# Kernel tuning notes

Measured on AMD Instinct MI355X. Metric: run time of the kernel, lower is better.

## Reference

```python
import jax, jax.numpy as jnp
import numpy as np

B, NG, GS, H = 256, 3008, 10, 6          # batch, n_genes, genes per leaf term, hidden per term
T = [2048, 256, 32, 1]                    # terms per DAG level (leaves -> root)
IN = [GS, 8 * H, 8 * H, 32 * H]           # per-term input size at each level
EPS = 1e-5


def setup_inputs() -> dict:
    keys = iter(jax.random.split(jax.random.key(0), 64))

    def rn(shape, s=0.1):
        return jax.random.normal(next(keys), shape, dtype=jnp.float32) * s

    d = {"x": rn((B, NG), 1.0),
         "gW": rn((T[0], GS, NG)),   # stacked leaf direct_gene_layer weights
         "gb": rn((T[0], GS))}
    for l in range(4):
        t, i = T[l], IN[l]
        d[f"w{l}"] = rn((t, H, i))          # term linear weight
        d[f"b{l}"] = rn((t, H))             # term linear bias
        d[f"g{l}"] = jnp.ones((t, H), jnp.float32)   # BN gamma
        d[f"e{l}"] = jnp.zeros((t, H), jnp.float32)  # BN beta
        d[f"p{l}"] = rn((t, H))             # aux linear1 weight (H->1)
        d[f"q{l}"] = rn((t,))               # aux linear1 bias
        d[f"r{l}"] = rn((t,))               # aux linear2 weight (1->1)
        d[f"s{l}"] = rn((t,))               # aux linear2 bias
    d["fw"] = rn((2 * H, H)); d["fb"] = rn((2 * H,))
    d["fg"] = jnp.ones((2 * H,), jnp.float32); d["fe"] = jnp.zeros((2 * H,), jnp.float32)
    d["pw"] = rn((1, 2 * H)); d["pb"] = rn((1,))
    d["rw"] = rn((1, 1)); d["rb"] = rn((1,))
    return d


def _bn(z, g, b):
    # BatchNorm1d in training mode: biased batch stats over axis 0
    m = z.mean(0)
    v = ((z - m) ** 2).mean(0)
    return (z - m) * jax.lax.rsqrt(v + EPS) * g + b


def reference(x, gW, gb,
              w0, b0, g0, e0, p0, q0, r0, s0,
              w1, b1, g1, e1, p1, q1, r1, s1,
              w2, b2, g2, e2, p2, q2, r2, s2,
              w3, b3, g3, e3, p3, q3, r3, s3,
              fw, fb, fg, fe, pw, pb, rw, rb):
    Bn = x.shape[0]
    # stacked direct gene layers for all leaf terms: [B, T0, GS]
    h = jnp.einsum('bn,tgn->btg', x, gW) + gb
    levels = [(w0, b0, g0, e0, p0, q0, r0, s0),
              (w1, b1, g1, e1, p1, q1, r1, s1),
              (w2, b2, g2, e2, p2, q2, r2, s2),
              (w3, b3, g3, e3, p3, q3, r3, s3)]
    aux = []
    for (w, b, g, e, p, q, r, s) in levels:
        # children of term t are contiguous -> concat == reshape
        hin = h.reshape(Bn, w.shape[0], w.shape[2])      # [B, T_l, in_l]
        z = jnp.tanh(jnp.einsum('bti,thi->bth', hin, w) + b)
        y = _bn(z, g, e)                                  # term_NN_out_map
        aux.append(r * jnp.tanh(jnp.einsum('bth,th->bt', y, p) + q) + s)
        h = y
    yroot = h.reshape(Bn, H)                              # root output [B, H]
    of = _bn(jnp.tanh(yroot @ fw.T + fb), fg, fe)         # final BN [B, 2H]
    auxf = jnp.tanh(of @ pw.T + pb) @ rw.T + rb           # final aux [B, 1]
    return jnp.concatenate(aux + [auxf], axis=1)          # [B, 2048+256+32+1+1]
```

## Files before the change

### kernel.cpp

```cpp
#include <hip/hip_runtime.h>
#include <hip/hip_bf16.h>
#include <stdint.h>

#define EPS 1e-5f
#define NOUT 2338

typedef __bf16 bf16x8 __attribute__((ext_vector_type(8)));
typedef float f32x4 __attribute__((ext_vector_type(4)));
typedef unsigned short u16;

__device__ __forceinline__ u16 f2bf_bits(float f) {
  uint32_t u = __builtin_bit_cast(uint32_t, f);
  u += 0x7FFFu + ((u >> 16) & 1u);
  return (u16)(u >> 16);
}

__device__ __forceinline__ uint32_t pack2(float lo, float hi) {
  return (uint32_t)f2bf_bits(lo) | ((uint32_t)f2bf_bits(hi) << 16);
}

__global__ __launch_bounds__(256) void cvt_pack_kernel(const float* __restrict__ x,
                                                       u16* __restrict__ xbp) {
  const int i = blockIdx.x * 256 + threadIdx.x;
  const int ks = i >> 10;
  const int rem = i & 1023;
  const int kb = rem >> 8;
  const int m = rem & 255;
  const f32x4* src = (const f32x4*)(x + (size_t)m * 3008 + ks * 32 + kb * 8);
  f32x4 a = src[0], b = src[1];
  uint4 o;
  o.x = pack2(a.x, a.y);
  o.y = pack2(a.z, a.w);
  o.z = pack2(b.x, b.y);
  o.w = pack2(b.z, b.w);
  ((uint4*)xbp)[i] = o;
}

__global__ __launch_bounds__(256, 3) void gemm_leaf(const float* __restrict__ W,
                                                    const float* __restrict__ gb,
                                                    const u16* __restrict__ XBp,
                                                    float* __restrict__ hout) {
  __shared__ __align__(16) u16 xl[2][8192];
  __shared__ __align__(16) float wlds[2][2048];
  const int tid = threadIdx.x;
  const int w = tid >> 6;
  const int lane = tid & 63;
  const int rh = w >> 1;
  const int mh = w & 1;
  const int lquad = lane >> 4;
  const int lmod = lane & 15;
  const int n0 = (blockIdx.x >> 1) * 64;
  const int kh = blockIdx.x & 1;
  const int kbase = kh * 47;

  f32x4 acc[2][8];
#pragma unroll
  for (int a = 0; a < 2; ++a)
#pragma unroll
    for (int j = 0; j < 8; ++j) acc[a][j] = (f32x4){0.f, 0.f, 0.f, 0.f};

  const u16* xsrc = XBp + (size_t)(w * 4) * 512 + lane * 8;
#define STAGE_X(ks, buf)                                                                \
  {                                                                                     \
    _Pragma("unroll")                                                                   \
    for (int p = 0; p < 4; ++p) {                                                       \
      const u16* src = xsrc + (size_t)(ks) * 8192 + p * 512 * 4;                        \
      u16* dst = &xl[buf][(w * 4 + p * 4) * 512];                                       \
      (void)src; (void)dst;                                                             \
    }                                                                                   \
  }
#undef STAGE_X

#define STAGE_X(ks, buf)                                                                \
  {                                                                                     \
    _Pragma("unroll")                                                                   \
    for (int p = 0; p < 4; ++p) {                                                       \
      const int c = (w * 4 + p) * 64;                                                   \
      const u16* src = XBp + (size_t)(ks) * 8192 + (size_t)(c + lane) * 8;              \
      u16* dst = &xl[buf][(size_t)c * 8];                                               \
      __builtin_amdgcn_global_load_lds((const __attribute__((address_space(1))) void*)src, \
                                       (__attribute__((address_space(3))) void*)dst,    \
                                       16, 0, 0);                                       \
    }                                                                                   \
  }

  const int wr0 = w * 2, wr1 = w * 2 + 1;
  const int lrow = lane >> 3;
  const int lswf = ((((lane & 7) * 16) ^ (lrow << 4)) >> 2);
  const float* wsrc0 = W + (size_t)(n0 + wr0 * 8 + lrow) * 3008 + lswf;
  const float* wsrc1 = W + (size_t)(n0 + wr1 * 8 + lrow) * 3008 + lswf;
#define STAGE_W(ks, buf)                                                                \
  {                                                                                     \
    __builtin_amdgcn_global_load_lds(                                                   \
        (const __attribute__((address_space(1))) void*)(wsrc0 + (size_t)(ks) * 32),     \
        (__attribute__((address_space(3))) void*)&wlds[buf][wr0 * 256], 16, 0, 0);      \
    __builtin_amdgcn_global_load_lds(                                                   \
        (const __attribute__((address_space(1))) void*)(wsrc1 + (size_t)(ks) * 32),     \
        (__attribute__((address_space(3))) void*)&wlds[buf][wr1 * 256], 16, 0, 0);      \
  }

  STAGE_X(kbase, 0);
  STAGE_W(kbase, 0);

  const int xorv = (lmod & 7) << 4;
  for (int s = 0; s < 47; ++s) {
    const int buf = s & 1;
    __syncthreads();
    if (s < 46) {
      STAGE_X(kbase + s + 1, buf ^ 1);
      STAGE_W(kbase + s + 1, buf ^ 1);
    }
    __builtin_amdgcn_sched_barrier(0);

    const float* wbase = &wlds[buf][0];
    const u16* xb = &xl[buf][(size_t)lquad * 2048 + mh * 1024 + lmod * 8];
    union { u16 u[8]; bf16x8 v; } af[2];
#pragma unroll
    for (int a = 0; a < 2; ++a) {
      const int row = rh * 32 + a * 16 + lmod;
      const int fb = row * 32;
      const f32x4 wlo = *(const f32x4*)(wbase + fb + (((lquad * 32) ^ xorv) >> 2));
      const f32x4 whi = *(const f32x4*)(wbase + fb + (((lquad * 32 + 16) ^ xorv) >> 2));
      af[a].u[0] = f2bf_bits(wlo.x); af[a].u[1] = f2bf_bits(wlo.y);
      af[a].u[2] = f2bf_bits(wlo.z); af[a].u[3] = f2bf_bits(wlo.w);
      af[a].u[4] = f2bf_bits(whi.x); af[a].u[5] = f2bf_bits(whi.y);
      af[a].u[6] = f2bf_bits(whi.z); af[a].u[7] = f2bf_bits(whi.w);
    }
#pragma unroll
    for (int j = 0; j < 8; ++j) {
      const bf16x8 bfrag = *(const bf16x8*)(xb + j * 128);
      acc[0][j] = __builtin_amdgcn_mfma_f32_16x16x32_bf16(af[0].v, bfrag, acc[0][j], 0, 0, 0);
      acc[1][j] = __builtin_amdgcn_mfma_f32_16x16x32_bf16(af[1].v, bfrag, acc[1][j], 0, 0, 0);
    }
  }

#undef STAGE_W
#undef STAGE_X

  float* hp = hout + (size_t)kh * 20480 * 256;
#pragma unroll
  for (int a = 0; a < 2; ++a) {
    const int r0 = n0 + rh * 32 + a * 16 + lquad * 4;
    float gb4[4];
#pragma unroll
    for (int r2 = 0; r2 < 4; ++r2) gb4[r2] = (kh == 0) ? gb[r0 + r2] : 0.f;
#pragma unroll
    for (int j = 0; j < 8; ++j) {
      const int col = (mh * 8 + j) * 16 + lmod;
#pragma unroll
      for (int r2 = 0; r2 < 4; ++r2) {
        hp[(size_t)(r0 + r2) * 256 + col] = acc[a][j][r2] + gb4[r2];
      }
    }
  }
}

__global__ __launch_bounds__(256) void level0_kernel(
    const float* __restrict__ yinA, const float* __restrict__ yinB,
    const float* __restrict__ w,
    const float* __restrict__ bia, const float* __restrict__ gam,
    const float* __restrict__ bet, const float* __restrict__ p,
    const float* __restrict__ q, const float* __restrict__ r,
    const float* __restrict__ s, float* __restrict__ yout,
    float* __restrict__ out, int inl, int off) {
  const int t = blockIdx.x;
  const int b = threadIdx.x;
  __shared__ float wls[6 * 10];
  __shared__ float part[4][12];
  __shared__ float stats[12];
  const float* wt = w + (size_t)t * 6 * inl;
  for (int i = b; i < 6 * inl; i += 256) wls[i] = wt[i];
  __syncthreads();

  float z[6];
#pragma unroll
  for (int h = 0; h < 6; ++h) z[h] = bia[t * 6 + h];
  const float* ypA = yinA + (size_t)t * inl * 256 + b;
  const float* ypB = yinB + (size_t)t * inl * 256 + b;
  for (int i = 0; i < inl; ++i) {
    float v = ypA[(size_t)i * 256] + ypB[(size_t)i * 256];
#pragma unroll
    for (int h = 0; h < 6; ++h) z[h] = fmaf(v, wls[h * inl + i], z[h]);
  }
#pragma unroll
  for (int h = 0; h < 6; ++h) z[h] = tanhf(z[h]);

  float sm[6], sq[6];
#pragma unroll
  for (int h = 0; h < 6; ++h) { sm[h] = z[h]; sq[h] = z[h] * z[h]; }
#pragma unroll
  for (int o = 32; o > 0; o >>= 1) {
#pragma unroll
    for (int h = 0; h < 6; ++h) {
      sm[h] += __shfl_down(sm[h], o);
      sq[h] += __shfl_down(sq[h], o);
    }
  }
  const int lane = b & 63, wvi = b >> 6;
  if (lane == 0) {
#pragma unroll
    for (int h = 0; h < 6; ++h) { part[wvi][h] = sm[h]; part[wvi][6 + h] = sq[h]; }
  }
  __syncthreads();
  if (b < 6) {
    float msum = part[0][b] + part[1][b] + part[2][b] + part[3][b];
    float qsum = part[0][6 + b] + part[1][6 + b] + part[2][6 + b] + part[3][6 + b];
    float m = msum * (1.f / 256.f);
    float var = qsum * (1.f / 256.f) - m * m;
    stats[b] = m;
    stats[6 + b] = rsqrtf(var + EPS);
  }
  __syncthreads();

  float a = q[t];
#pragma unroll
  for (int h = 0; h < 6; ++h) {
    float yy = (z[h] - stats[h]) * stats[6 + h] * gam[t * 6 + h] + bet[t * 6 + h];
    yout[((size_t)t * 6 + h) * 256 + b] = yy;
    a = fmaf(yy, p[t * 6 + h], a);
  }
  out[(size_t)b * NOUT + off + t] = tanhf(a) * r[t] + s[t];
}

__global__ __launch_bounds__(256) void level_kernel(
    const float* __restrict__ yin, const float* __restrict__ w,
    const float* __restrict__ bia, const float* __restrict__ gam,
    const float* __restrict__ bet, const float* __restrict__ p,
    const float* __restrict__ q, const float* __restrict__ r,
    const float* __restrict__ s, float* __restrict__ yout,
    float* __restrict__ out, int inl, int off) {
  const int t = blockIdx.x;
  const int b = threadIdx.x;
  __shared__ float wls[6 * 48];
  __shared__ float part[4][12];
  __shared__ float stats[12];
  const float* wt = w + (size_t)t * 6 * inl;
  for (int i = b; i < 6 * inl; i += 256) wls[i] = wt[i];
  __syncthreads();

  float z[6];
#pragma unroll
  for (int h = 0; h < 6; ++h) z[h] = bia[t * 6 + h];
  const float* yp = yin + (size_t)t * inl * 256 + b;
  for (int i = 0; i < inl; ++i) {
    float v = yp[(size_t)i * 256];
#pragma unroll
    for (int h = 0; h < 6; ++h) z[h] = fmaf(v, wls[h * inl + i], z[h]);
  }
#pragma unroll
  for (int h = 0; h < 6; ++h) z[h] = tanhf(z[h]);

  float sm[6], sq[6];
#pragma unroll
  for (int h = 0; h < 6; ++h) { sm[h] = z[h]; sq[h] = z[h] * z[h]; }
#pragma unroll
  for (int o = 32; o > 0; o >>= 1) {
#pragma unroll
    for (int h = 0; h < 6; ++h) {
      sm[h] += __shfl_down(sm[h], o);
      sq[h] += __shfl_down(sq[h], o);
    }
  }
  const int lane = b & 63, wvi = b >> 6;
  if (lane == 0) {
#pragma unroll
    for (int h = 0; h < 6; ++h) { part[wvi][h] = sm[h]; part[wvi][6 + h] = sq[h]; }
  }
  __syncthreads();
  if (b < 6) {
    float msum = part[0][b] + part[1][b] + part[2][b] + part[3][b];
    float qsum = part[0][6 + b] + part[1][6 + b] + part[2][6 + b] + part[3][6 + b];
    float m = msum * (1.f / 256.f);
    float var = qsum * (1.f / 256.f) - m * m;
    stats[b] = m;
    stats[6 + b] = rsqrtf(var + EPS);
  }
  __syncthreads();

  float a = q[t];
#pragma unroll
  for (int h = 0; h < 6; ++h) {
    float yy = (z[h] - stats[h]) * stats[6 + h] * gam[t * 6 + h] + bet[t * 6 + h];
    yout[((size_t)t * 6 + h) * 256 + b] = yy;
    a = fmaf(yy, p[t * 6 + h], a);
  }
  out[(size_t)b * NOUT + off + t] = tanhf(a) * r[t] + s[t];
}

__global__ __launch_bounds__(256) void level3_final_kernel(
    const float* __restrict__ y2,
    const float* __restrict__ w3, const float* __restrict__ b3,
    const float* __restrict__ g3, const float* __restrict__ e3,
    const float* __restrict__ p3, const float* __restrict__ q3,
    const float* __restrict__ r3, const float* __restrict__ s3,
    const float* __restrict__ fw, const float* __restrict__ fb,
    const float* __restrict__ fg, const float* __restrict__ fe,
    const float* __restrict__ pw, const float* __restrict__ pb,
    const float* __restrict__ rw, const float* __restrict__ rb,
    float* __restrict__ out) {
  const int b = threadIdx.x;
  __shared__ float wls[6 * 192];
  __shared__ float part[4][24];
  __shared__ float stats[24];
  for (int i = b; i < 6 * 192; i += 256) wls[i] = w3[i];
  __syncthreads();

  float z[6];
#pragma unroll
  for (int h = 0; h < 6; ++h) z[h] = b3[h];
  const float* yp = y2 + b;
  for (int i = 0; i < 192; ++i) {
    float v = yp[(size_t)i * 256];
#pragma unroll
    for (int h = 0; h < 6; ++h) z[h] = fmaf(v, wls[h * 192 + i], z[h]);
  }
#pragma unroll
  for (int h = 0; h < 6; ++h) z[h] = tanhf(z[h]);

  const int lane = b & 63, wvi = b >> 6;
  {
    float sm[6], sq[6];
#pragma unroll
    for (int h = 0; h < 6; ++h) { sm[h] = z[h]; sq[h] = z[h] * z[h]; }
#pragma unroll
    for (int o = 32; o > 0; o >>= 1) {
#pragma unroll
      for (int h = 0; h < 6; ++h) {
        sm[h] += __shfl_down(sm[h], o);
        sq[h] += __shfl_down(sq[h], o);
      }
    }
    if (lane == 0) {
#pragma unroll
      for (int h = 0; h < 6; ++h) { part[wvi][h] = sm[h]; part[wvi][6 + h] = sq[h]; }
    }
    __syncthreads();
    if (b < 6) {
      float msum = part[0][b] + part[1][b] + part[2][b] + part[3][b];
      float qsum = part[0][6 + b] + part[1][6 + b] + part[2][6 + b] + part[3][6 + b];
      float m = msum * (1.f / 256.f);
      float var = qsum * (1.f / 256.f) - m * m;
      stats[b] = m;
      stats[6 + b] = rsqrtf(var + EPS);
    }
    __syncthreads();
  }

  float yr[6];
  float a3 = q3[0];
#pragma unroll
  for (int h = 0; h < 6; ++h) {
    yr[h] = (z[h] - stats[h]) * stats[6 + h] * g3[h] + e3[h];
    a3 = fmaf(yr[h], p3[h], a3);
  }
  out[(size_t)b * NOUT + 2336] = tanhf(a3) * r3[0] + s3[0];
  __syncthreads();

  float zf[12];
#pragma unroll
  for (int j = 0; j < 12; ++j) {
    float a = fb[j];
#pragma unroll
    for (int h = 0; h < 6; ++h) a = fmaf(yr[h], fw[j * 6 + h], a);
    zf[j] = tanhf(a);
  }
  {
    float sm[12], sq[12];
#pragma unroll
    for (int j = 0; j < 12; ++j) { sm[j] = zf[j]; sq[j] = zf[j] * zf[j]; }
#pragma unroll
    for (int o = 32; o > 0; o >>= 1) {
#pragma unroll
      for (int j = 0; j < 12; ++j) {
        sm[j] += __shfl_down(sm[j], o);
        sq[j] += __shfl_down(sq[j], o);
      }
    }
    if (lane == 0) {
#pragma unroll
      for (int j = 0; j < 12; ++j) { part[wvi][j] = sm[j]; part[wvi][12 + j] = sq[j]; }
    }
    __syncthreads();
    if (b < 12) {
      float msum = part[0][b] + part[1][b] + part[2][b] + part[3][b];
      float qsum = part[0][12 + b] + part[1][12 + b] + part[2][12 + b] + part[3][12 + b];
      float m = msum * (1.f / 256.f);
      float var = qsum * (1.f / 256.f) - m * m;
      stats[b] = m;
      stats[12 + b] = rsqrtf(var + EPS);
    }
    __syncthreads();
  }
  float a = pb[0];
#pragma unroll
  for (int j = 0; j < 12; ++j) {
    float of = (zf[j] - stats[j]) * stats[12 + j] * fg[j] + fe[j];
    a = fmaf(of, pw[j], a);
  }
  out[(size_t)b * NOUT + 2337] = tanhf(a) * rw[0] + rb[0];
}

extern "C" void kernel_launch(void* const* d_in, const int* in_sizes, int n_in,
                              void* d_out, int out_size, void* d_ws, size_t ws_size,
                              hipStream_t stream) {
  const float* x  = (const float*)d_in[0];
  const float* gW = (const float*)d_in[1];
  const float* gb = (const float*)d_in[2];
  float* out = (float*)d_out;

  char* wsb = (char*)d_ws;
  u16* XBp = (u16*)wsb;
  float* h0 = (float*)(wsb + 1540096);
  float* y0 = h0 + (size_t)2 * 20480 * 256;
  float* y1 = y0 + (size_t)12288 * 256;
  float* y2 = y1 + (size_t)1536 * 256;

  cvt_pack_kernel<<<dim3(376), dim3(256), 0, stream>>>(x, XBp);
  gemm_leaf<<<dim3(640), dim3(256), 0, stream>>>(gW, gb, XBp, h0);

  level0_kernel<<<dim3(2048), dim3(256), 0, stream>>>(
      h0, h0 + (size_t)20480 * 256,
      (const float*)d_in[3], (const float*)d_in[4], (const float*)d_in[5],
      (const float*)d_in[6], (const float*)d_in[7], (const float*)d_in[8],
      (const float*)d_in[9], (const float*)d_in[10], y0, out, 10, 0);

#define LV(base, yin, yout, inl, off, grid)                                           \
  level_kernel<<<dim3(grid), dim3(256), 0, stream>>>(                                 \
      yin, (const float*)d_in[base], (const float*)d_in[base + 1],                    \
      (const float*)d_in[base + 2], (const float*)d_in[base + 3],                     \
      (const float*)d_in[base + 4], (const float*)d_in[base + 5],                     \
      (const float*)d_in[base + 6], (const float*)d_in[base + 7], yout, out, inl, off)

  LV(11, y0, y1, 48,  2048, 256);
  LV(19, y1, y2, 48,  2304, 32);
#undef LV

  level3_final_kernel<<<dim3(1), dim3(256), 0, stream>>>(
      y2,
      (const float*)d_in[27], (const float*)d_in[28], (const float*)d_in[29],
      (const float*)d_in[30], (const float*)d_in[31], (const float*)d_in[32],
      (const float*)d_in[33], (const float*)d_in[34],
      (const float*)d_in[35], (const float*)d_in[36], (const float*)d_in[37],
      (const float*)d_in[38], (const float*)d_in[39], (const float*)d_in[40],
      (const float*)d_in[41], (const float*)d_in[42], out);
}
```

Measured before the change: 137.9 us.

## Enlarge leaf GEMM row tile to 128 and split K four ways

The leaf gene GEMM now has each block compute 128 output rows instead of 64, reusing each staged X tile across twice as many weight rows. K is split into four partitions instead of two so the grid stays at 640 blocks. The level-0 kernel now sums the four partial outputs. In exchange the kernel uses more registers and LDS (occupancy hint lowered from 3 to 2), and the partial-sum buffer written and read back to global memory doubles in size.

```diff
diff --git a/kernel.cpp b/kernel.cpp
--- a/kernel.cpp
+++ b/kernel.cpp
@@ -36,12 +36,12 @@
   ((uint4*)xbp)[i] = o;
 }
 
-__global__ __launch_bounds__(256, 3) void gemm_leaf(const float* __restrict__ W,
+__global__ __launch_bounds__(256, 2) void gemm_leaf(const float* __restrict__ W,
                                                     const float* __restrict__ gb,
                                                     const u16* __restrict__ XBp,
                                                     float* __restrict__ hout) {
   __shared__ __align__(16) u16 xl[2][8192];
-  __shared__ __align__(16) float wlds[2][2048];
+  __shared__ __align__(16) float wlds[2][4096];
   const int tid = threadIdx.x;
   const int w = tid >> 6;
   const int lane = tid & 63;
@@ -49,27 +49,16 @@
   const int mh = w & 1;
   const int lquad = lane >> 4;
   const int lmod = lane & 15;
-  const int n0 = (blockIdx.x >> 1) * 64;
-  const int kh = blockIdx.x & 1;
-  const int kbase = kh * 47;
-
-  f32x4 acc[2][8];
-#pragma unroll
-  for (int a = 0; a < 2; ++a)
+  const int n0 = (blockIdx.x >> 2) * 128;
+  const int kh = blockIdx.x & 3;
+  const int kbase = kh * 24 - ((kh > 2) ? (kh - 2) : 0);
+  const int nst = 24 - ((kh >= 2) ? 1 : 0);
+
+  f32x4 acc[4][8];
+#pragma unroll
+  for (int a = 0; a < 4; ++a)
 #pragma unroll
     for (int j = 0; j < 8; ++j) acc[a][j] = (f32x4){0.f, 0.f, 0.f, 0.f};
-
-  const u16* xsrc = XBp + (size_t)(w * 4) * 512 + lane * 8;
-#define STAGE_X(ks, buf)                                                                \
-  {                                                                                     \
-    _Pragma("unroll")                                                                   \
-    for (int p = 0; p < 4; ++p) {                                                       \
-      const u16* src = xsrc + (size_t)(ks) * 8192 + p * 512 * 4;                        \
-      u16* dst = &xl[buf][(w * 4 + p * 4) * 512];                                       \
-      (void)src; (void)dst;                                                             \
-    }                                                                                   \
-  }
-#undef STAGE_X
 
 #define STAGE_X(ks, buf)                                                                \
   {                                                                                     \
@@ -84,53 +73,55 @@
     }                                                                                   \
   }
 
-  const int wr0 = w * 2, wr1 = w * 2 + 1;
   const int lrow = lane >> 3;
   const int lswf = ((((lane & 7) * 16) ^ (lrow << 4)) >> 2);
-  const float* wsrc0 = W + (size_t)(n0 + wr0 * 8 + lrow) * 3008 + lswf;
-  const float* wsrc1 = W + (size_t)(n0 + wr1 * 8 + lrow) * 3008 + lswf;
 #define STAGE_W(ks, buf)                                                                \
   {                                                                                     \
-    __builtin_amdgcn_global_load_lds(                                                   \
-        (const __attribute__((address_space(1))) void*)(wsrc0 + (size_t)(ks) * 32),     \
-        (__attribute__((address_space(3))) void*)&wlds[buf][wr0 * 256], 16, 0, 0);      \
-    __builtin_amdgcn_global_load_lds(                                                   \
-        (const __attribute__((address_space(1))) void*)(wsrc1 + (size_t)(ks) * 32),     \
-        (__attribute__((address_space(3))) void*)&wlds[buf][wr1 * 256], 16, 0, 0);      \
+    _Pragma("unroll")                                                                   \
+    for (int p = 0; p < 4; ++p) {                                                       \
+      const int q = w * 4 + p;                                                          \
+      const float* src = W + (size_t)(n0 + q * 8 + lrow) * 3008 + (size_t)(ks) * 32 + lswf; \
+      float* dst = &wlds[buf][q * 256];                                                 \
+      __builtin_amdgcn_global_load_lds((const __attribute__((address_space(1))) void*)src, \
+                                       (__attribute__((address_space(3))) void*)dst,    \
+                                       16, 0, 0);                                       \
+    }                                                                                   \
   }
 
   STAGE_X(kbase, 0);
   STAGE_W(kbase, 0);
 
   const int xorv = (lmod & 7) << 4;
-  for (int s = 0; s < 47; ++s) {
+  for (int s = 0; s < nst; ++s) {
     const int buf = s & 1;
     __syncthreads();
-    if (s < 46) {
+    if (s + 1 < nst) {
       STAGE_X(kbase + s + 1, buf ^ 1);
       STAGE_W(kbase + s + 1, buf ^ 1);
     }
     __builtin_amdgcn_sched_barrier(0);
 
+    const u16* xb = &xl[buf][(size_t)lquad * 2048 + mh * 1024 + lmod * 8];
+    bf16x8 B[8];
+#pragma unroll
+    for (int j = 0; j < 8; ++j) B[j] = *(const bf16x8*)(xb + j * 128);
+
     const float* wbase = &wlds[buf][0];
-    const u16* xb = &xl[buf][(size_t)lquad * 2048 + mh * 1024 + lmod * 8];
-    union { u16 u[8]; bf16x8 v; } af[2];
-#pragma unroll
-    for (int a = 0; a < 2; ++a) {
-      const int row = rh * 32 + a * 16 + lmod;
+#pragma unroll
+    for (int a = 0; a < 4; ++a) {
+      const int row = rh * 64 + a * 16 + lmod;
       const int fb = row * 32;
       const f32x4 wlo = *(const f32x4*)(wbase + fb + (((lquad * 32) ^ xorv) >> 2));
       const f32x4 whi = *(const f32x4*)(wbase + fb + (((lquad * 32 + 16) ^ xorv) >> 2));
-      af[a].u[0] = f2bf_bits(wlo.x); af[a].u[1] = f2bf_bits(wlo.y);
-      af[a].u[2] = f2bf_bits(wlo.z); af[a].u[3] = f2bf_bits(wlo.w);
-      af[a].u[4] = f2bf_bits(whi.x); af[a].u[5] = f2bf_bits(whi.y);
-      af[a].u[6] = f2bf_bits(whi.z); af[a].u[7] = f2bf_bits(whi.w);
-    }
-#pragma unroll
-    for (int j = 0; j < 8; ++j) {
-      const bf16x8 bfrag = *(const bf16x8*)(xb + j * 128);
-      acc[0][j] = __builtin_amdgcn_mfma_f32_16x16x32_bf16(af[0].v, bfrag, acc[0][j], 0, 0, 0);
-      acc[1][j] = __builtin_amdgcn_mfma_f32_16x16x32_bf16(af[1].v, bfrag, acc[1][j], 0, 0, 0);
+      union { u16 u[8]; bf16x8 v; } af;
+      af.u[0] = f2bf_bits(wlo.x); af.u[1] = f2bf_bits(wlo.y);
+      af.u[2] = f2bf_bits(wlo.z); af.u[3] = f2bf_bits(wlo.w);
+      af.u[4] = f2bf_bits(whi.x); af.u[5] = f2bf_bits(whi.y);
+      af.u[6] = f2bf_bits(whi.z); af.u[7] = f2bf_bits(whi.w);
+#pragma unroll
+      for (int j = 0; j < 8; ++j) {
+        acc[a][j] = __builtin_amdgcn_mfma_f32_16x16x32_bf16(af.v, B[j], acc[a][j], 0, 0, 0);
+      }
     }
   }
 
@@ -139,8 +130,8 @@
 
   float* hp = hout + (size_t)kh * 20480 * 256;
 #pragma unroll
-  for (int a = 0; a < 2; ++a) {
-    const int r0 = n0 + rh * 32 + a * 16 + lquad * 4;
+  for (int a = 0; a < 4; ++a) {
+    const int r0 = n0 + rh * 64 + a * 16 + lquad * 4;
     float gb4[4];
 #pragma unroll
     for (int r2 = 0; r2 < 4; ++r2) gb4[r2] = (kh == 0) ? gb[r0 + r2] : 0.f;
@@ -156,8 +147,7 @@
 }
 
 __global__ __launch_bounds__(256) void level0_kernel(
-    const float* __restrict__ yinA, const float* __restrict__ yinB,
-    const float* __restrict__ w,
+    const float* __restrict__ yin, const float* __restrict__ w,
     const float* __restrict__ bia, const float* __restrict__ gam,
     const float* __restrict__ bet, const float* __restrict__ p,
     const float* __restrict__ q, const float* __restrict__ r,
@@ -165,6 +155,7 @@
     float* __restrict__ out, int inl, int off) {
   const int t = blockIdx.x;
   const int b = threadIdx.x;
+  const size_t P = (size_t)20480 * 256;
   __shared__ float wls[6 * 10];
   __shared__ float part[4][12];
   __shared__ float stats[12];
@@ -175,10 +166,10 @@
   float z[6];
 #pragma unroll
   for (int h = 0; h < 6; ++h) z[h] = bia[t * 6 + h];
-  const float* ypA = yinA + (size_t)t * inl * 256 + b;
-  const float* ypB = yinB + (size_t)t * inl * 256 + b;
+  const float* yp = yin + (size_t)t * inl * 256 + b;
   for (int i = 0; i < inl; ++i) {
-    float v = ypA[(size_t)i * 256] + ypB[(size_t)i * 256];
+    const size_t o = (size_t)i * 256;
+    float v = yp[o] + yp[P + o] + yp[2 * P + o] + yp[3 * P + o];
 #pragma unroll
     for (int h = 0; h < 6; ++h) z[h] = fmaf(v, wls[h * inl + i], z[h]);
   }
@@ -411,7 +402,7 @@
   char* wsb = (char*)d_ws;
   u16* XBp = (u16*)wsb;
   float* h0 = (float*)(wsb + 1540096);
-  float* y0 = h0 + (size_t)2 * 20480 * 256;
+  float* y0 = h0 + (size_t)4 * 20480 * 256;
   float* y1 = y0 + (size_t)12288 * 256;
   float* y2 = y1 + (size_t)1536 * 256;
 
@@ -419,7 +410,7 @@
   gemm_leaf<<<dim3(640), dim3(256), 0, stream>>>(gW, gb, XBp, h0);
 
   level0_kernel<<<dim3(2048), dim3(256), 0, stream>>>(
-      h0, h0 + (size_t)20480 * 256,
+      h0,
       (const float*)d_in[3], (const float*)d_in[4], (const float*)d_in[5],
       (const float*)d_in[6], (const float*)d_in[7], (const float*)d_in[8],
       (const float*)d_in[9], (const float*)d_in[10], y0, out, 10, 0);
```

After: 156.1 us. +13.2%, slower.
